# Kernel tuning notes

Hardware: AMD Instinct MI355X
Metric: run time of the kernel (lower is better)

## Reference

```python
import jax, jax.numpy as jnp
import numpy as np

N = 100000   # nodes
E = 1600000  # edges
IN, HID, OUT = 128, 128, 64

def setup_inputs() -> dict:
    key = jax.random.key(0)
    ks = jax.random.split(key, 18)
    def lin(k, i, o):
        kw, kb = jax.random.split(k)
        s = 1.0 / np.sqrt(i)
        return (jax.random.uniform(kw, (i, o), jnp.float32, -s, s),
                jax.random.uniform(kb, (o,), jnp.float32, -s, s))
    x = jax.random.normal(ks[0], (N, IN), jnp.float32)
    edge_index = jax.random.randint(ks[1], (2, E), 0, N, jnp.int64)
    W1, b1   = lin(ks[2], IN, HID)
    W21, b21 = lin(ks[3], IN, HID)
    W22, b22 = lin(ks[4], HID, HID)
    W31, b31 = lin(ks[5], IN, HID)
    W32, b32 = lin(ks[6], HID, HID)
    W33, b33 = lin(ks[7], HID, HID)
    Wa, ba   = lin(ks[8], HID, 1)
    Wf, bf   = lin(ks[9], HID, OUT)
    return dict(x=x, edge_index=edge_index, W1=W1, b1=b1, W21=W21, b21=b21,
                W22=W22, b22=b22, W31=W31, b31=b31, W32=W32, b32=b32,
                W33=W33, b33=b33, Wa=Wa, ba=ba, Wf=Wf, bf=bf)

def _gcn(x, W, b, src, dst, dinv):
    # PyG GCNConv: D^{-1/2}(A+I)D^{-1/2} X W + b, self-loops added.
    h = x @ W                                    # [N, F]
    norm = dinv[src] * dinv[dst]                 # [E]
    agg = jax.ops.segment_sum(h[src] * norm[:, None], dst, num_segments=N)
    agg = agg + h * (dinv * dinv)[:, None]       # self-loop contribution
    return agg + b

def reference(x, edge_index, W1, b1, W21, b21, W22, b22, W31, b31,
              W32, b32, W33, b33, Wa, ba, Wf, bf):
    src, dst = edge_index[0], edge_index[1]
    # degree with self-loops (in-degree at target nodes)
    deg = jax.ops.segment_sum(jnp.ones(E, x.dtype), dst, num_segments=N) + 1.0
    dinv = jax.lax.rsqrt(deg)
    h1 = jax.nn.relu(_gcn(x, W1, b1, src, dst, dinv))
    h2 = jax.nn.relu(_gcn(x, W21, b21, src, dst, dinv))
    h2 = jax.nn.relu(_gcn(h2, W22, b22, src, dst, dinv))
    h3 = jax.nn.relu(_gcn(x, W31, b31, src, dst, dinv))
    h3 = jax.nn.relu(_gcn(h3, W32, b32, src, dst, dinv))
    h3 = jax.nn.relu(_gcn(h3, W33, b33, src, dst, dinv))
    H = jnp.stack([h1, h2, h3], axis=1)          # [N, 3, HID]
    scores = H @ Wa + ba                         # [N, 3, 1]
    w = jax.nn.softmax(scores, axis=1)
    h_meta = jnp.sum(w * H, axis=1)              # [N, HID]
    h_out = h_meta + h1
    return h_out @ Wf + bf                       # [N, OUT]
```

## Files before the change

### kernel.cpp

```cpp
#include <hip/hip_runtime.h>
#include <hip/hip_bf16.h>

#define HIDF 128
#define OUTF 64
#define SCAN_B 256
#define BK_SHIFT 7

typedef __attribute__((ext_vector_type(8))) short bf16x8;
typedef __attribute__((ext_vector_type(4))) float f32x4;

__device__ __forceinline__ float us2f(unsigned u_lo16) {
    return __uint_as_float(u_lo16 << 16);
}
__device__ __forceinline__ float hi2f(unsigned u) {
    return __uint_as_float(u & 0xffff0000u);
}
__device__ __forceinline__ unsigned short f2us(float f) {
    __hip_bfloat16 h = __float2bfloat16(f);
    return *reinterpret_cast<unsigned short*>(&h);
}
__device__ __forceinline__ unsigned pack2(float a, float b) {
    return (unsigned)f2us(a) | ((unsigned)f2us(b) << 16);
}

__global__ __launch_bounds__(256) void deg_zero(int* __restrict__ d, int N) {
    int i = blockIdx.x * 256 + threadIdx.x;
    if (i < N) d[i] = 0;
}

__global__ __launch_bounds__(256) void deg_count(const int* __restrict__ ei, int* __restrict__ d, int E) {
    int e = blockIdx.x * 256 + threadIdx.x;
    if (e < E) atomicAdd(&d[ei[E + e]], 1);
}

__global__ __launch_bounds__(256) void scanA(const int* __restrict__ degi, int* __restrict__ blocksum, int N) {
    __shared__ int red[256];
    const int b = blockIdx.x;
    const int chunk = (N + SCAN_B - 1) / SCAN_B;
    const int lo = b * chunk, hi = min(lo + chunk, N);
    int s = 0;
    for (int i = lo + threadIdx.x; i < hi; i += 256) s += degi[i];
    red[threadIdx.x] = s;
    __syncthreads();
    for (int off = 128; off; off >>= 1) {
        if (threadIdx.x < off) red[threadIdx.x] += red[threadIdx.x + off];
        __syncthreads();
    }
    if (threadIdx.x == 0) blocksum[b] = red[0];
}

__global__ __launch_bounds__(256) void scanB(const int* __restrict__ blocksum, int* __restrict__ blockoff) {
    __shared__ int ps[256];
    const int t = threadIdx.x;
    ps[t] = blocksum[t];
    __syncthreads();
    for (int off = 1; off < 256; off <<= 1) {
        int v = ps[t];
        int u = (t >= off) ? ps[t - off] : 0;
        __syncthreads();
        ps[t] = v + u;
        __syncthreads();
    }
    blockoff[t] = (t == 0) ? 0 : ps[t - 1];
}

__global__ __launch_bounds__(256) void scanC(const int* __restrict__ degi,
                                             const int* __restrict__ blockoff,
                                             int* __restrict__ cursor,
                                             float* __restrict__ dinv, int N) {
    __shared__ int ps[256];
    const int b = blockIdx.x;
    const int chunk = (N + SCAN_B - 1) / SCAN_B;
    const int lo = b * chunk, hi = min(lo + chunk, N);
    const int tchunk = (chunk + 255) / 256;
    const int tlo = lo + threadIdx.x * tchunk;
    const int thi = min(tlo + tchunk, hi);
    int s = 0;
    for (int i = tlo; i < thi; ++i) s += degi[i];
    ps[threadIdx.x] = s;
    __syncthreads();
    for (int off = 1; off < 256; off <<= 1) {
        int v = ps[threadIdx.x];
        int u = (threadIdx.x >= off) ? ps[threadIdx.x - off] : 0;
        __syncthreads();
        ps[threadIdx.x] = v + u;
        __syncthreads();
    }
    int base = blockoff[b] + ((threadIdx.x == 0) ? 0 : ps[threadIdx.x - 1]);
    for (int i = tlo; i < thi; ++i) {
        int d = degi[i];
        cursor[i] = base;
        base += d;
        dinv[i] = rsqrtf((float)d + 1.f);
    }
}

__global__ __launch_bounds__(256) void bcur_init(const int* __restrict__ cursor,
                                                 int* __restrict__ bcur, int N, int NBK) {
    int b = blockIdx.x * 256 + threadIdx.x;
    if (b < NBK) bcur[b * 64] = cursor[b << BK_SHIFT];
}

__global__ __launch_bounds__(256) void bucket_scatter(const int* __restrict__ ei,
                                                      int* __restrict__ bcur,
                                                      unsigned* __restrict__ edg, int E) {
    int e = blockIdx.x * 256 + threadIdx.x;
    if (e >= E) return;
    int src = ei[e];
    int dst = ei[E + e];
    int pos = atomicAdd(&bcur[(dst >> BK_SHIFT) * 64], 1);
    edg[pos] = ((unsigned)src << BK_SHIFT) | (unsigned)(dst & ((1 << BK_SHIFT) - 1));
}

__global__ __launch_bounds__(256) void final_scatter_b(const unsigned* __restrict__ edg,
                                                       const int* __restrict__ bcur,
                                                       int* __restrict__ cursor,
                                                       int* __restrict__ csr_src) {
    const int b = blockIdx.x;
    __shared__ int sstart;
    if (threadIdx.x == 0) sstart = cursor[b << BK_SHIFT];
    __syncthreads();
    const int bstart = sstart;
    const int bend   = bcur[b * 64];
    const int base   = b << BK_SHIFT;
    for (int p = bstart + threadIdx.x; p < bend; p += 256) {
        unsigned u = edg[p];
        int src = (int)(u >> BK_SHIFT);
        int dst = base | (int)(u & ((1u << BK_SHIFT) - 1));
        int pos = atomicAdd(&cursor[dst], 1);
        csr_src[pos] = src;
    }
}

__global__ __launch_bounds__(256) void cvt_scale(const float* __restrict__ X,
                                                 const float* __restrict__ dinv,
                                                 unsigned short* __restrict__ TB, int N) {
    int g = blockIdx.x * 256 + threadIdx.x;
    if (g >= N * 32) return;
    int n = g >> 5;
    float dv = dinv[n];
    float4 v = ((const float4*)X)[g];
    ushort4 o;
    o.x = f2us(v.x * dv); o.y = f2us(v.y * dv);
    o.z = f2us(v.z * dv); o.w = f2us(v.w * dv);
    ((ushort4*)TB)[g] = o;
}

__global__ __launch_bounds__(256) void cvt_w(const float* __restrict__ Wa0,
                                             const float* __restrict__ Wa1,
                                             const float* __restrict__ Wa2,
                                             const float* __restrict__ Wa3,
                                             const float* __restrict__ Wa4,
                                             const float* __restrict__ Wa5,
                                             unsigned short* __restrict__ WTB) {
    int t = blockIdx.x * 256 + threadIdx.x;
    if (t >= 6 * 16384) return;
    int m = t >> 14, local = t & 16383;
    int n = local >> 7, k = local & 127;
    const float* src = (m == 0) ? Wa0 : (m == 1) ? Wa1 : (m == 2) ? Wa2
                     : (m == 3) ? Wa3 : (m == 4) ? Wa4 : Wa5;
    WTB[t] = f2us(src[k * 128 + n]);
}

__global__ __launch_bounds__(256) void agg_b2(const unsigned short* __restrict__ TB,
                                              const float* __restrict__ dinv,
                                              const int* __restrict__ csr_src,
                                              const int* __restrict__ rend,
                                              unsigned* __restrict__ O, int N) {
    const int n = (blockIdx.x * 256 + threadIdx.x) >> 6;
    const int l = threadIdx.x & 63;
    if (n >= N) return;
    const int half = l >> 5;
    const int sl   = l & 31;
    const int start = (n == 0) ? 0 : rend[n - 1];
    const int end   = rend[n];
    const uint2* Tv = (const uint2*)TB;

    float a0 = 0.f, a1 = 0.f, a2 = 0.f, a3 = 0.f;
    int e = start;
    for (; e + 8 <= end; e += 8) {
        int sA = csr_src[e + 0 + half];
        int sB = csr_src[e + 2 + half];
        int sC = csr_src[e + 4 + half];
        int sD = csr_src[e + 6 + half];
        uint2 vA = Tv[(size_t)sA * 32 + sl];
        uint2 vB = Tv[(size_t)sB * 32 + sl];
        uint2 vC = Tv[(size_t)sC * 32 + sl];
        uint2 vD = Tv[(size_t)sD * 32 + sl];
        a0 += us2f(vA.x & 0xffffu); a1 += hi2f(vA.x); a2 += us2f(vA.y & 0xffffu); a3 += hi2f(vA.y);
        a0 += us2f(vB.x & 0xffffu); a1 += hi2f(vB.x); a2 += us2f(vB.y & 0xffffu); a3 += hi2f(vB.y);
        a0 += us2f(vC.x & 0xffffu); a1 += hi2f(vC.x); a2 += us2f(vC.y & 0xffffu); a3 += hi2f(vC.y);
        a0 += us2f(vD.x & 0xffffu); a1 += hi2f(vD.x); a2 += us2f(vD.y & 0xffffu); a3 += hi2f(vD.y);
    }
    for (; e + 2 <= end; e += 2) {
        int s = csr_src[e + half];
        uint2 v = Tv[(size_t)s * 32 + sl];
        a0 += us2f(v.x & 0xffffu); a1 += hi2f(v.x); a2 += us2f(v.y & 0xffffu); a3 += hi2f(v.y);
    }
    if (e < end && half == 0) {
        int s = csr_src[e];
        uint2 v = Tv[(size_t)s * 32 + sl];
        a0 += us2f(v.x & 0xffffu); a1 += hi2f(v.x); a2 += us2f(v.y & 0xffffu); a3 += hi2f(v.y);
    }
    if (half == 0) {
        uint2 v = Tv[(size_t)n * 32 + sl];
        a0 += us2f(v.x & 0xffffu); a1 += hi2f(v.x); a2 += us2f(v.y & 0xffffu); a3 += hi2f(v.y);
    }
    a0 += __shfl_xor(a0, 32); a1 += __shfl_xor(a1, 32);
    a2 += __shfl_xor(a2, 32); a3 += __shfl_xor(a3, 32);
    if (half == 0) {
        const float dv = dinv[n];
        uint2 o;
        o.x = pack2(a0 * dv, a1 * dv);
        o.y = pack2(a2 * dv, a3 * dv);
        ((uint2*)O)[(size_t)n * 32 + sl] = o;
    }
}

__global__ __launch_bounds__(256) void agg_dual2(const unsigned short* __restrict__ TB23,
                                                 const float* __restrict__ dinv,
                                                 const int* __restrict__ csr_src,
                                                 const int* __restrict__ rend,
                                                 unsigned* __restrict__ OA,
                                                 unsigned* __restrict__ OB, int N) {
    const int n = (blockIdx.x * 256 + threadIdx.x) >> 6;
    const int l = threadIdx.x & 63;
    if (n >= N) return;
    const int start = (n == 0) ? 0 : rend[n - 1];
    const int end   = rend[n];
    const uint2* Tv = (const uint2*)TB23;

    float a0 = 0.f, a1 = 0.f, a2 = 0.f, a3 = 0.f;
    int e = start;
    for (; e + 4 <= end; e += 4) {
        int s0 = csr_src[e + 0], s1 = csr_src[e + 1], s2 = csr_src[e + 2], s3 = csr_src[e + 3];
        uint2 v0 = Tv[(size_t)s0 * 64 + l];
        uint2 v1 = Tv[(size_t)s1 * 64 + l];
        uint2 v2 = Tv[(size_t)s2 * 64 + l];
        uint2 v3 = Tv[(size_t)s3 * 64 + l];
        a0 += us2f(v0.x & 0xffffu); a1 += hi2f(v0.x); a2 += us2f(v0.y & 0xffffu); a3 += hi2f(v0.y);
        a0 += us2f(v1.x & 0xffffu); a1 += hi2f(v1.x); a2 += us2f(v1.y & 0xffffu); a3 += hi2f(v1.y);
        a0 += us2f(v2.x & 0xffffu); a1 += hi2f(v2.x); a2 += us2f(v2.y & 0xffffu); a3 += hi2f(v2.y);
        a0 += us2f(v3.x & 0xffffu); a1 += hi2f(v3.x); a2 += us2f(v3.y & 0xffffu); a3 += hi2f(v3.y);
    }
    for (; e < end; ++e) {
        int s = csr_src[e];
        uint2 v = Tv[(size_t)s * 64 + l];
        a0 += us2f(v.x & 0xffffu); a1 += hi2f(v.x); a2 += us2f(v.y & 0xffffu); a3 += hi2f(v.y);
    }
    {
        uint2 v = Tv[(size_t)n * 64 + l];
        a0 += us2f(v.x & 0xffffu); a1 += hi2f(v.x); a2 += us2f(v.y & 0xffffu); a3 += hi2f(v.y);
    }
    const float dv = dinv[n];
    uint2 o;
    o.x = pack2(a0 * dv, a1 * dv);
    o.y = pack2(a2 * dv, a3 * dv);
    if (l < 32) ((uint2*)OA)[(size_t)n * 32 + l] = o;
    else        ((uint2*)OB)[(size_t)n * 32 + (l - 32)] = o;
}

#define OM_F32 0
#define OM_BF16 1
#define OM_BF16_SR 2
template <int OMODE, int OSTRIDE>
__global__ __launch_bounds__(256) void gemm_mfma(const unsigned short* __restrict__ Xb,
                                                 const unsigned short* __restrict__ WT,
                                                 const float* __restrict__ bias,
                                                 const float* __restrict__ dinv,
                                                 void* __restrict__ T, int N) {
    __shared__ unsigned short Xs[64 * 128];
    __shared__ unsigned short Ws[128 * 128];
    const int tid = threadIdx.x;
    const int nb = blockIdx.x * 64;

    for (int c = tid; c < 2048; c += 256) {
        int n = c >> 4, kc = c & 15;
        ((uint4*)Ws)[(n << 4) | (kc ^ (n & 7))] = ((const uint4*)WT)[c];
    }
    for (int c = tid; c < 1024; c += 256) {
        int nl = c >> 4, kc = c & 15;
        int n = nb + nl;
        uint4 v = make_uint4(0u, 0u, 0u, 0u);
        if (n < N) v = ((const uint4*)(Xb + (size_t)n * HIDF))[kc];
        ((uint4*)Xs)[(nl << 4) | (kc ^ (nl & 7))] = v;
    }
    __syncthreads();

    const int wv   = tid >> 6;
    const int l    = tid & 63;
    const int row  = l & 15;
    const int kgrp = l >> 4;

    bf16x8 afr[4];
    #pragma unroll
    for (int kk = 0; kk < 4; ++kk) {
        int nl = 16 * wv + row;
        int kc = kk * 4 + kgrp;
        afr[kk] = *(const bf16x8*)(Xs + nl * 128 + ((kc ^ (nl & 7)) << 3));
    }

    f32x4 acc[8];
    #pragma unroll
    for (int nt = 0; nt < 8; ++nt) {
        float b = bias[nt * 16 + row];
        acc[nt] = (f32x4){b, b, b, b};
    }

    #pragma unroll
    for (int nt = 0; nt < 8; ++nt) {
        int col = nt * 16 + row;
        #pragma unroll
        for (int kk = 0; kk < 4; ++kk) {
            int kc = kk * 4 + kgrp;
            bf16x8 bfr = *(const bf16x8*)(Ws + col * 128 + ((kc ^ (col & 7)) << 3));
            acc[nt] = __builtin_amdgcn_mfma_f32_16x16x32_bf16(afr[kk], bfr, acc[nt], 0, 0, 0);
        }
    }

    float dv[4];
    if (OMODE == OM_BF16_SR) {
        #pragma unroll
        for (int r = 0; r < 4; ++r) {
            int grow = nb + 16 * wv + kgrp * 4 + r;
            dv[r] = (grow < N) ? dinv[grow] : 0.f;
        }
    }
    #pragma unroll
    for (int nt = 0; nt < 8; ++nt) {
        int gcol = nt * 16 + row;
        #pragma unroll
        for (int r = 0; r < 4; ++r) {
            int grow = nb + 16 * wv + kgrp * 4 + r;
            if (grow < N) {
                float v = acc[nt][r];
                if (OMODE == OM_BF16_SR) v = fmaxf(v, 0.f) * dv[r];
                if (OMODE == OM_F32) {
                    ((float*)T)[(size_t)grow * OSTRIDE + gcol] = v;
                } else {
                    ((unsigned short*)T)[(size_t)grow * OSTRIDE + gcol] = f2us(v);
                }
            }
        }
    }
}

__global__ __launch_bounds__(256) void meta_kernel(const float* __restrict__ H1,
                                                   const unsigned* __restrict__ H2B,
                                                   const unsigned* __restrict__ H3B,
                                                   const float* __restrict__ Wa,
                                                   const float* __restrict__ ba,
                                                   const float* __restrict__ Wf,
                                                   const float* __restrict__ bfb,
                                                   float* __restrict__ out, int N) {
    __shared__ float WfS[HIDF * OUTF];
    __shared__ float WaS[HIDF];
    __shared__ float hm[4][HIDF];
    const int tid = threadIdx.x;
    for (int i = tid; i < HIDF * OUTF; i += 256) WfS[i] = Wf[i];
    if (tid < HIDF) WaS[tid] = Wa[tid];
    __syncthreads();
    const float bav = ba[0];
    const int w = tid >> 6;
    const int l = tid & 63;
    const float bfv = bfb[l];
    const int iters = (N + 3) >> 2;

    for (int it = blockIdx.x; it < iters; it += gridDim.x) {
        const int n = it * 4 + w;
        __syncthreads();
        if (n < N) {
            float2   p1 = ((const float2*)(H1 + (size_t)n * HIDF))[l];
            unsigned u2 = H2B[(size_t)n * 64 + l];
            unsigned u3 = H3B[(size_t)n * 64 + l];
            float h1a = fmaxf(p1.x, 0.f),              h1b = fmaxf(p1.y, 0.f);
            float h2a = fmaxf(us2f(u2 & 0xffffu), 0.f), h2b = fmaxf(hi2f(u2), 0.f);
            float h3a = fmaxf(us2f(u3 & 0xffffu), 0.f), h3b = fmaxf(hi2f(u3), 0.f);
            float wa0 = WaS[2 * l], wa1 = WaS[2 * l + 1];
            float s1 = h1a * wa0 + h1b * wa1;
            float s2 = h2a * wa0 + h2b * wa1;
            float s3 = h3a * wa0 + h3b * wa1;
            #pragma unroll
            for (int off = 32; off; off >>= 1) {
                s1 += __shfl_xor(s1, off);
                s2 += __shfl_xor(s2, off);
                s3 += __shfl_xor(s3, off);
            }
            s1 += bav; s2 += bav; s3 += bav;
            float m  = fmaxf(s1, fmaxf(s2, s3));
            float e1 = expf(s1 - m), e2 = expf(s2 - m), e3 = expf(s3 - m);
            float inv = 1.f / (e1 + e2 + e3);
            float w1 = e1 * inv, w2 = e2 * inv, w3 = e3 * inv;
            hm[w][2 * l]     = w1 * h1a + w2 * h2a + w3 * h3a + h1a;
            hm[w][2 * l + 1] = w1 * h1b + w2 * h2b + w3 * h3b + h1b;
        }
        __syncthreads();
        if (n < N) {
            float acc = bfv;
            #pragma unroll
            for (int k = 0; k < HIDF; ++k) acc = fmaf(hm[w][k], WfS[k * OUTF + l], acc);
            out[(size_t)n * OUTF + l] = acc;
        }
    }
}

extern "C" void kernel_launch(void* const* d_in, const int* in_sizes, int n_in,
                              void* d_out, int out_size, void* d_ws, size_t ws_size,
                              hipStream_t stream) {
    const float* x   = (const float*)d_in[0];
    const int*   ei  = (const int*)d_in[1];
    const float *W1  = (const float*)d_in[2],  *b1  = (const float*)d_in[3];
    const float *W21 = (const float*)d_in[4],  *b21 = (const float*)d_in[5];
    const float *W22 = (const float*)d_in[6],  *b22 = (const float*)d_in[7];
    const float *W31 = (const float*)d_in[8],  *b31 = (const float*)d_in[9];
    const float *W32 = (const float*)d_in[10], *b32 = (const float*)d_in[11];
    const float *W33 = (const float*)d_in[12], *b33 = (const float*)d_in[13];
    const float *Wa  = (const float*)d_in[14], *ba  = (const float*)d_in[15];
    const float *Wf  = (const float*)d_in[16], *bfb = (const float*)d_in[17];

    const int N = in_sizes[0] / HIDF;
    const int E = in_sizes[1] / 2;
    const int NBK = (N + 127) >> BK_SHIFT;

    int*      DEGI    = (int*)d_ws;
    int*      CURSOR  = DEGI + N;
    int*      CSR_SRC = CURSOR + N;
    unsigned* EDG     = (unsigned*)(CSR_SRC + E);
    int*      BCUR    = (int*)(EDG + E);
    int*      BSUM    = BCUR + 1024 * 64;
    int*      BOFF    = BSUM + 256;
    float*    DINV    = (float*)(BOFF + 256);
    unsigned short* TB23 = (unsigned short*)(DINV + N);
    unsigned* PXB  = (unsigned*)(TB23 + (size_t)N * 256);
    unsigned* AGA  = PXB + (size_t)N * 64;
    unsigned* AGB  = AGA + (size_t)N * 64;
    unsigned* H2B  = AGB + (size_t)N * 64;
    unsigned short* WTB = (unsigned short*)(H2B + (size_t)N * 64);

    const int gN    = (N + 255) / 256;
    const int gE    = (E + 255) / 256;
    const int gCVT  = (N * 32 + 255) / 256;
    const int gAGG  = (N * 64 + 255) / 256;
    const int gGEMM = (N + 63) / 64;
    const int gMETA = 2048;

    deg_zero<<<gN, 256, 0, stream>>>(DEGI, N);
    deg_count<<<gE, 256, 0, stream>>>(ei, DEGI, E);
    scanA<<<SCAN_B, 256, 0, stream>>>(DEGI, BSUM, N);
    scanB<<<1, 256, 0, stream>>>(BSUM, BOFF);
    scanC<<<SCAN_B, 256, 0, stream>>>(DEGI, BOFF, CURSOR, DINV, N);
    bcur_init<<<(NBK + 255) / 256, 256, 0, stream>>>(CURSOR, BCUR, N, NBK);
    bucket_scatter<<<gE, 256, 0, stream>>>(ei, BCUR, EDG, E);
    final_scatter_b<<<NBK, 256, 0, stream>>>(EDG, BCUR, CURSOR, CSR_SRC);
    cvt_w<<<384, 256, 0, stream>>>(W21, W31, W22, W32, W33, W1, WTB);

    unsigned short* TBX = TB23;

    cvt_scale<<<gCVT, 256, 0, stream>>>(x, DINV, TBX, N);
    agg_b2<<<gAGG, 256, 0, stream>>>(TBX, DINV, CSR_SRC, CURSOR, PXB, N);

    gemm_mfma<OM_BF16_SR, 256><<<gGEMM, 256, 0, stream>>>((unsigned short*)PXB, WTB,         b21, DINV, TB23,       N);
    gemm_mfma<OM_BF16_SR, 256><<<gGEMM, 256, 0, stream>>>((unsigned short*)PXB, WTB + 16384, b31, DINV, TB23 + 128, N);
    agg_dual2<<<gAGG, 256, 0, stream>>>(TB23, DINV, CSR_SRC, CURSOR, AGA, AGB, N);

    gemm_mfma<OM_BF16, 128><<<gGEMM, 256, 0, stream>>>((unsigned short*)AGA, WTB + 2 * 16384, b22, DINV, H2B, N);
    gemm_mfma<OM_BF16_SR, 128><<<gGEMM, 256, 0, stream>>>((unsigned short*)AGB, WTB + 3 * 16384, b32, DINV, TBX, N);
    agg_b2<<<gAGG, 256, 0, stream>>>(TBX, DINV, CSR_SRC, CURSOR, AGA, N);
    gemm_mfma<OM_BF16, 128><<<gGEMM, 256, 0, stream>>>((unsigned short*)AGA, WTB + 4 * 16384, b33, DINV, AGB, N);

    float* H1F = (float*)TB23;
    gemm_mfma<OM_F32, 128><<<gGEMM, 256, 0, stream>>>((unsigned short*)PXB, WTB + 5 * 16384, b1, DINV, H1F, N);

    meta_kernel<<<gMETA, 256, 0, stream>>>(H1F, H2B, AGB, Wa, ba, Wf, bfb,
                                           (float*)d_out, N);
}
```

Measured before the change: 705.8 us.

## Build CSR via bucket histogram and per-bucket LDS counting; unroll gather loops

Replaces the per-node degree atomics plus three-stage scan with a per-bucket histogram (padded counters), a single-block bucket scan, and a per-bucket kernel that computes node degrees, row ends and dinv in shared memory before placing edges using LDS atomics. This removes several launches and the global per-node atomics in the final scatter. It also deepens the unroll of the aggregation gather loops (16 edges in agg_b2, 8 in the other) to keep more loads in flight, at the cost of register pressure.

```diff
diff --git a/kernel.cpp b/kernel.cpp
--- a/kernel.cpp
+++ b/kernel.cpp
@@ -3,7 +3,6 @@
 
 #define HIDF 128
 #define OUTF 64
-#define SCAN_B 256
 #define BK_SHIFT 7
 
 typedef __attribute__((ext_vector_type(8))) short bf16x8;
@@ -23,82 +22,34 @@
     return (unsigned)f2us(a) | ((unsigned)f2us(b) << 16);
 }
 
-__global__ __launch_bounds__(256) void deg_zero(int* __restrict__ d, int N) {
+__global__ __launch_bounds__(256) void bhist_zero(int* __restrict__ bs, int total) {
     int i = blockIdx.x * 256 + threadIdx.x;
-    if (i < N) d[i] = 0;
-}
-
-__global__ __launch_bounds__(256) void deg_count(const int* __restrict__ ei, int* __restrict__ d, int E) {
+    if (i < total) bs[i] = 0;
+}
+
+__global__ __launch_bounds__(256) void bhist_count(const int* __restrict__ ei,
+                                                   int* __restrict__ bs, int E) {
     int e = blockIdx.x * 256 + threadIdx.x;
-    if (e < E) atomicAdd(&d[ei[E + e]], 1);
-}
-
-__global__ __launch_bounds__(256) void scanA(const int* __restrict__ degi, int* __restrict__ blocksum, int N) {
-    __shared__ int red[256];
-    const int b = blockIdx.x;
-    const int chunk = (N + SCAN_B - 1) / SCAN_B;
-    const int lo = b * chunk, hi = min(lo + chunk, N);
-    int s = 0;
-    for (int i = lo + threadIdx.x; i < hi; i += 256) s += degi[i];
-    red[threadIdx.x] = s;
-    __syncthreads();
-    for (int off = 128; off; off >>= 1) {
-        if (threadIdx.x < off) red[threadIdx.x] += red[threadIdx.x + off];
-        __syncthreads();
-    }
-    if (threadIdx.x == 0) blocksum[b] = red[0];
-}
-
-__global__ __launch_bounds__(256) void scanB(const int* __restrict__ blocksum, int* __restrict__ blockoff) {
-    __shared__ int ps[256];
+    if (e < E) atomicAdd(&bs[(ei[E + e] >> BK_SHIFT) * 16], 1);
+}
+
+__global__ __launch_bounds__(1024) void bscan(const int* __restrict__ bs,
+                                              int* __restrict__ bstart,
+                                              int* __restrict__ bcur, int NBK, int E) {
+    __shared__ int ps[1024];
     const int t = threadIdx.x;
-    ps[t] = blocksum[t];
-    __syncthreads();
-    for (int off = 1; off < 256; off <<= 1) {
+    ps[t] = (t < NBK) ? bs[t * 16] : 0;
+    __syncthreads();
+    for (int off = 1; off < 1024; off <<= 1) {
         int v = ps[t];
         int u = (t >= off) ? ps[t - off] : 0;
         __syncthreads();
         ps[t] = v + u;
         __syncthreads();
     }
-    blockoff[t] = (t == 0) ? 0 : ps[t - 1];
-}
-
-__global__ __launch_bounds__(256) void scanC(const int* __restrict__ degi,
-                                             const int* __restrict__ blockoff,
-                                             int* __restrict__ cursor,
-                                             float* __restrict__ dinv, int N) {
-    __shared__ int ps[256];
-    const int b = blockIdx.x;
-    const int chunk = (N + SCAN_B - 1) / SCAN_B;
-    const int lo = b * chunk, hi = min(lo + chunk, N);
-    const int tchunk = (chunk + 255) / 256;
-    const int tlo = lo + threadIdx.x * tchunk;
-    const int thi = min(tlo + tchunk, hi);
-    int s = 0;
-    for (int i = tlo; i < thi; ++i) s += degi[i];
-    ps[threadIdx.x] = s;
-    __syncthreads();
-    for (int off = 1; off < 256; off <<= 1) {
-        int v = ps[threadIdx.x];
-        int u = (threadIdx.x >= off) ? ps[threadIdx.x - off] : 0;
-        __syncthreads();
-        ps[threadIdx.x] = v + u;
-        __syncthreads();
-    }
-    int base = blockoff[b] + ((threadIdx.x == 0) ? 0 : ps[threadIdx.x - 1]);
-    for (int i = tlo; i < thi; ++i) {
-        int d = degi[i];
-        cursor[i] = base;
-        base += d;
-        dinv[i] = rsqrtf((float)d + 1.f);
-    }
-}
-
-__global__ __launch_bounds__(256) void bcur_init(const int* __restrict__ cursor,
-                                                 int* __restrict__ bcur, int N, int NBK) {
-    int b = blockIdx.x * 256 + threadIdx.x;
-    if (b < NBK) bcur[b * 64] = cursor[b << BK_SHIFT];
+    int ex = (t == 0) ? 0 : ps[t - 1];
+    if (t < NBK) { bstart[t] = ex; bcur[t * 64] = ex; }
+    if (t == 0) bstart[NBK] = E;
 }
 
 __global__ __launch_bounds__(256) void bucket_scatter(const int* __restrict__ ei,
@@ -112,23 +63,47 @@
     edg[pos] = ((unsigned)src << BK_SHIFT) | (unsigned)(dst & ((1 << BK_SHIFT) - 1));
 }
 
-__global__ __launch_bounds__(256) void final_scatter_b(const unsigned* __restrict__ edg,
-                                                       const int* __restrict__ bcur,
-                                                       int* __restrict__ cursor,
-                                                       int* __restrict__ csr_src) {
+__global__ __launch_bounds__(256) void csr_build(const unsigned* __restrict__ edg,
+                                                 const int* __restrict__ bstart,
+                                                 int* __restrict__ rend,
+                                                 int* __restrict__ csr_src,
+                                                 float* __restrict__ dinv, int N) {
     const int b = blockIdx.x;
-    __shared__ int sstart;
-    if (threadIdx.x == 0) sstart = cursor[b << BK_SHIFT];
-    __syncthreads();
-    const int bstart = sstart;
-    const int bend   = bcur[b * 64];
-    const int base   = b << BK_SHIFT;
-    for (int p = bstart + threadIdx.x; p < bend; p += 256) {
+    const int lo = bstart[b], hi = bstart[b + 1];
+    const int base = b << BK_SHIFT;
+    __shared__ int hist[128], curs[128], ps[128];
+    if (threadIdx.x < 128) hist[threadIdx.x] = 0;
+    __syncthreads();
+    for (int p = lo + threadIdx.x; p < hi; p += 256)
+        atomicAdd(&hist[edg[p] & 127], 1);
+    __syncthreads();
+    if (threadIdx.x < 128) ps[threadIdx.x] = hist[threadIdx.x];
+    __syncthreads();
+    for (int off = 1; off < 128; off <<= 1) {
+        int v = 0;
+        if (threadIdx.x < 128) {
+            v = ps[threadIdx.x];
+            if (threadIdx.x >= off) v += ps[threadIdx.x - off];
+        }
+        __syncthreads();
+        if (threadIdx.x < 128) ps[threadIdx.x] = v;
+        __syncthreads();
+    }
+    if (threadIdx.x < 128) {
+        int n = base + threadIdx.x;
+        if (n < N) {
+            int inc = ps[threadIdx.x];
+            int d   = hist[threadIdx.x];
+            rend[n] = lo + inc;
+            curs[threadIdx.x] = lo + inc - d;
+            dinv[n] = rsqrtf((float)d + 1.f);
+        }
+    }
+    __syncthreads();
+    for (int p = lo + threadIdx.x; p < hi; p += 256) {
         unsigned u = edg[p];
-        int src = (int)(u >> BK_SHIFT);
-        int dst = base | (int)(u & ((1u << BK_SHIFT) - 1));
-        int pos = atomicAdd(&cursor[dst], 1);
-        csr_src[pos] = src;
+        int pos = atomicAdd(&curs[u & 127], 1);
+        csr_src[pos] = (int)(u >> BK_SHIFT);
     }
 }
 
@@ -178,11 +153,31 @@
 
     float a0 = 0.f, a1 = 0.f, a2 = 0.f, a3 = 0.f;
     int e = start;
-    for (; e + 8 <= end; e += 8) {
-        int sA = csr_src[e + 0 + half];
-        int sB = csr_src[e + 2 + half];
-        int sC = csr_src[e + 4 + half];
-        int sD = csr_src[e + 6 + half];
+    for (; e + 16 <= end; e += 16) {
+        int sA = csr_src[e +  0 + half], sB = csr_src[e +  2 + half];
+        int sC = csr_src[e +  4 + half], sD = csr_src[e +  6 + half];
+        int sE = csr_src[e +  8 + half], sF = csr_src[e + 10 + half];
+        int sG = csr_src[e + 12 + half], sH = csr_src[e + 14 + half];
+        uint2 vA = Tv[(size_t)sA * 32 + sl];
+        uint2 vB = Tv[(size_t)sB * 32 + sl];
+        uint2 vC = Tv[(size_t)sC * 32 + sl];
+        uint2 vD = Tv[(size_t)sD * 32 + sl];
+        uint2 vE = Tv[(size_t)sE * 32 + sl];
+        uint2 vF = Tv[(size_t)sF * 32 + sl];
+        uint2 vG = Tv[(size_t)sG * 32 + sl];
+        uint2 vH = Tv[(size_t)sH * 32 + sl];
+        a0 += us2f(vA.x & 0xffffu); a1 += hi2f(vA.x); a2 += us2f(vA.y & 0xffffu); a3 += hi2f(vA.y);
+        a0 += us2f(vB.x & 0xffffu); a1 += hi2f(vB.x); a2 += us2f(vB.y & 0xffffu); a3 += hi2f(vB.y);
+        a0 += us2f(vC.x & 0xffffu); a1 += hi2f(vC.x); a2 += us2f(vC.y & 0xffffu); a3 += hi2f(vC.y);
+        a0 += us2f(vD.x & 0xffffu); a1 += hi2f(vD.x); a2 += us2f(vD.y & 0xffffu); a3 += hi2f(vD.y);
+        a0 += us2f(vE.x & 0xffffu); a1 += hi2f(vE.x); a2 += us2f(vE.y & 0xffffu); a3 += hi2f(vE.y);
+        a0 += us2f(vF.x & 0xffffu); a1 += hi2f(vF.x); a2 += us2f(vF.y & 0xffffu); a3 += hi2f(vF.y);
+        a0 += us2f(vG.x & 0xffffu); a1 += hi2f(vG.x); a2 += us2f(vG.y & 0xffffu); a3 += hi2f(vG.y);
+        a0 += us2f(vH.x & 0xffffu); a1 += hi2f(vH.x); a2 += us2f(vH.y & 0xffffu); a3 += hi2f(vH.y);
+    }
+    if (e + 8 <= end) {
+        int sA = csr_src[e + 0 + half], sB = csr_src[e + 2 + half];
+        int sC = csr_src[e + 4 + half], sD = csr_src[e + 6 + half];
         uint2 vA = Tv[(size_t)sA * 32 + sl];
         uint2 vB = Tv[(size_t)sB * 32 + sl];
         uint2 vC = Tv[(size_t)sC * 32 + sl];
@@ -191,6 +186,7 @@
         a0 += us2f(vB.x & 0xffffu); a1 += hi2f(vB.x); a2 += us2f(vB.y & 0xffffu); a3 += hi2f(vB.y);
         a0 += us2f(vC.x & 0xffffu); a1 += hi2f(vC.x); a2 += us2f(vC.y & 0xffffu); a3 += hi2f(vC.y);
         a0 += us2f(vD.x & 0xffffu); a1 += hi2f(vD.x); a2 += us2f(vD.y & 0xffffu); a3 += hi2f(vD.y);
+        e += 8;
     }
     for (; e + 2 <= end; e += 2) {
         int s = csr_src[e + half];
@@ -232,16 +228,25 @@
 
     float a0 = 0.f, a1 = 0.f, a2 = 0.f, a3 = 0.f;
     int e = start;
-    for (; e + 4 <= end; e += 4) {
+    for (; e + 8 <= end; e += 8) {
         int s0 = csr_src[e + 0], s1 = csr_src[e + 1], s2 = csr_src[e + 2], s3 = csr_src[e + 3];
+        int s4 = csr_src[e + 4], s5 = csr_src[e + 5], s6 = csr_src[e + 6], s7 = csr_src[e + 7];
         uint2 v0 = Tv[(size_t)s0 * 64 + l];
         uint2 v1 = Tv[(size_t)s1 * 64 + l];
         uint2 v2 = Tv[(size_t)s2 * 64 + l];
         uint2 v3 = Tv[(size_t)s3 * 64 + l];
+        uint2 v4 = Tv[(size_t)s4 * 64 + l];
+        uint2 v5 = Tv[(size_t)s5 * 64 + l];
+        uint2 v6 = Tv[(size_t)s6 * 64 + l];
+        uint2 v7 = Tv[(size_t)s7 * 64 + l];
         a0 += us2f(v0.x & 0xffffu); a1 += hi2f(v0.x); a2 += us2f(v0.y & 0xffffu); a3 += hi2f(v0.y);
         a0 += us2f(v1.x & 0xffffu); a1 += hi2f(v1.x); a2 += us2f(v1.y & 0xffffu); a3 += hi2f(v1.y);
         a0 += us2f(v2.x & 0xffffu); a1 += hi2f(v2.x); a2 += us2f(v2.y & 0xffffu); a3 += hi2f(v2.y);
         a0 += us2f(v3.x & 0xffffu); a1 += hi2f(v3.x); a2 += us2f(v3.y & 0xffffu); a3 += hi2f(v3.y);
+        a0 += us2f(v4.x & 0xffffu); a1 += hi2f(v4.x); a2 += us2f(v4.y & 0xffffu); a3 += hi2f(v4.y);
+        a0 += us2f(v5.x & 0xffffu); a1 += hi2f(v5.x); a2 += us2f(v5.y & 0xffffu); a3 += hi2f(v5.y);
+        a0 += us2f(v6.x & 0xffffu); a1 += hi2f(v6.x); a2 += us2f(v6.y & 0xffffu); a3 += hi2f(v6.y);
+        a0 += us2f(v7.x & 0xffffu); a1 += hi2f(v7.x); a2 += us2f(v7.y & 0xffffu); a3 += hi2f(v7.y);
     }
     for (; e < end; ++e) {
         int s = csr_src[e];
@@ -373,7 +378,7 @@
             float2   p1 = ((const float2*)(H1 + (size_t)n * HIDF))[l];
             unsigned u2 = H2B[(size_t)n * 64 + l];
             unsigned u3 = H3B[(size_t)n * 64 + l];
-            float h1a = fmaxf(p1.x, 0.f),              h1b = fmaxf(p1.y, 0.f);
+            float h1a = fmaxf(p1.x, 0.f),               h1b = fmaxf(p1.y, 0.f);
             float h2a = fmaxf(us2f(u2 & 0xffffu), 0.f), h2b = fmaxf(hi2f(u2), 0.f);
             float h3a = fmaxf(us2f(u3 & 0xffffu), 0.f), h3b = fmaxf(hi2f(u3), 0.f);
             float wa0 = WaS[2 * l], wa1 = WaS[2 * l + 1];
@@ -422,14 +427,13 @@
     const int E = in_sizes[1] / 2;
     const int NBK = (N + 127) >> BK_SHIFT;
 
-    int*      DEGI    = (int*)d_ws;
-    int*      CURSOR  = DEGI + N;
-    int*      CSR_SRC = CURSOR + N;
+    int*      REND    = (int*)d_ws;
+    int*      CSR_SRC = REND + N;
     unsigned* EDG     = (unsigned*)(CSR_SRC + E);
     int*      BCUR    = (int*)(EDG + E);
-    int*      BSUM    = BCUR + 1024 * 64;
-    int*      BOFF    = BSUM + 256;
-    float*    DINV    = (float*)(BOFF + 256);
+    int*      BSIZE   = BCUR + 1024 * 64;
+    int*      BSTART  = BSIZE + 1024 * 16;
+    float*    DINV    = (float*)(BSTART + 1040);
     unsigned short* TB23 = (unsigned short*)(DINV + N);
     unsigned* PXB  = (unsigned*)(TB23 + (size_t)N * 256);
     unsigned* AGA  = PXB + (size_t)N * 64;
@@ -437,35 +441,31 @@
     unsigned* H2B  = AGB + (size_t)N * 64;
     unsigned short* WTB = (unsigned short*)(H2B + (size_t)N * 64);
 
-    const int gN    = (N + 255) / 256;
     const int gE    = (E + 255) / 256;
     const int gCVT  = (N * 32 + 255) / 256;
     const int gAGG  = (N * 64 + 255) / 256;
     const int gGEMM = (N + 63) / 64;
     const int gMETA = 2048;
 
-    deg_zero<<<gN, 256, 0, stream>>>(DEGI, N);
-    deg_count<<<gE, 256, 0, stream>>>(ei, DEGI, E);
-    scanA<<<SCAN_B, 256, 0, stream>>>(DEGI, BSUM, N);
-    scanB<<<1, 256, 0, stream>>>(BSUM, BOFF);
-    scanC<<<SCAN_B, 256, 0, stream>>>(DEGI, BOFF, CURSOR, DINV, N);
-    bcur_init<<<(NBK + 255) / 256, 256, 0, stream>>>(CURSOR, BCUR, N, NBK);
+    bhist_zero<<<(NBK * 16 + 255) / 256, 256, 0, stream>>>(BSIZE, NBK * 16);
+    bhist_count<<<gE, 256, 0, stream>>>(ei, BSIZE, E);
+    bscan<<<1, 1024, 0, stream>>>(BSIZE, BSTART, BCUR, NBK, E);
     bucket_scatter<<<gE, 256, 0, stream>>>(ei, BCUR, EDG, E);
-    final_scatter_b<<<NBK, 256, 0, stream>>>(EDG, BCUR, CURSOR, CSR_SRC);
+    csr_build<<<NBK, 256, 0, stream>>>(EDG, BSTART, REND, CSR_SRC, DINV, N);
     cvt_w<<<384, 256, 0, stream>>>(W21, W31, W22, W32, W33, W1, WTB);
 
     unsigned short* TBX = TB23;
 
     cvt_scale<<<gCVT, 256, 0, stream>>>(x, DINV, TBX, N);
-    agg_b2<<<gAGG, 256, 0, stream>>>(TBX, DINV, CSR_SRC, CURSOR, PXB, N);
+    agg_b2<<<gAGG, 256, 0, stream>>>(TBX, DINV, CSR_SRC, REND, PXB, N);
 
     gemm_mfma<OM_BF16_SR, 256><<<gGEMM, 256, 0, stream>>>((unsigned short*)PXB, WTB,         b21, DINV, TB23,       N);
     gemm_mfma<OM_BF16_SR, 256><<<gGEMM, 256, 0, stream>>>((unsigned short*)PXB, WTB + 16384, b31, DINV, TB23 + 128, N);
-    agg_dual2<<<gAGG, 256, 0, stream>>>(TB23, DINV, CSR_SRC, CURSOR, AGA, AGB, N);
+    agg_dual2<<<gAGG, 256, 0, stream>>>(TB23, DINV, CSR_SRC, REND, AGA, AGB, N);
 
     gemm_mfma<OM_BF16, 128><<<gGEMM, 256, 0, stream>>>((unsigned short*)AGA, WTB + 2 * 16384, b22, DINV, H2B, N);
     gemm_mfma<OM_BF16_SR, 128><<<gGEMM, 256, 0, stream>>>((unsigned short*)AGB, WTB + 3 * 16384, b32, DINV, TBX, N);
-    agg_b2<<<gAGG, 256, 0, stream>>>(TBX, DINV, CSR_SRC, CURSOR, AGA, N);
+    agg_b2<<<gAGG, 256, 0, stream>>>(TBX, DINV, CSR_SRC, REND, AGA, N);
     gemm_mfma<OM_BF16, 128><<<gGEMM, 256, 0, stream>>>((unsigned short*)AGA, WTB + 4 * 16384, b33, DINV, AGB, N);
 
     float* H1F = (float*)TB23;
```

Result: slower. 755.0 us (+7.0%).
